# Optimization experiments

Hardware: AMD Instinct MI355X
Metric: run time of the kernel (lower is better)

Reference implementation:

```python
import jax, jax.numpy as jnp
import numpy as np

B, N, DIM, H, DH = 2, 4096, 512, 8, 64  # inner_dim = H*DH = 512


def setup_inputs() -> dict:
    key = jax.random.key(0)
    ks = jax.random.split(key, 4)
    x = jax.random.normal(ks[0], (B, N, DIM), dtype=jnp.float32)
    Wq = jax.random.normal(ks[1], (DIM, H * DH), dtype=jnp.float32) * (DIM ** -0.5)
    Wkv = jax.random.normal(ks[2], (DIM, 2 * H * DH), dtype=jnp.float32) * (DIM ** -0.5)
    Wo = jax.random.normal(ks[3], (H * DH, DIM), dtype=jnp.float32) * ((H * DH) ** -0.5)
    bo = jnp.zeros((DIM,), dtype=jnp.float32)
    return {"x": x, "Wq": Wq, "Wkv": Wkv, "Wo": Wo, "bo": bo}


def reference(x, Wq, Wkv, Wo, bo):
    scale = DH ** -0.5
    # projections (context defaults to x -> self-attention)
    q = x @ Wq
    kv = x @ Wkv
    k, v = jnp.split(kv, 2, axis=-1)
    # NOTE: original code scales q by dim_head**-0.5 in forward() AND again
    # inside attention(), i.e. an effective dim_head**-1 scaling. Faithful.
    q = q * scale
    # b n (h d) -> b h n d
    split_heads = lambda t: t.reshape(B, N, H, DH).transpose(0, 2, 1, 3)
    q, k, v = map(split_heads, (q, k, v))
    q = q * scale  # second scaling inside attention()
    sim = jnp.einsum('bhid,bhjd->bhij', q, k)  # [B,H,N,N] full score matrix
    sim = sim - jax.lax.stop_gradient(jnp.max(sim, axis=-1, keepdims=True))
    mask_value = -jnp.finfo(sim.dtype).max
    causal_mask = jnp.triu(jnp.ones((N, N), dtype=bool), k=1)
    sim = jnp.where(causal_mask, mask_value, sim)
    attn = jax.nn.softmax(sim, axis=-1)
    out = jnp.einsum('bhij,bhjd->bhid', attn, v)
    out = out.transpose(0, 2, 1, 3).reshape(B, N, H * DH)  # b h n d -> b n (h d)
    return out @ Wo + bo
```

## Files before the change

kernel.cpp:

```cpp
#include <hip/hip_runtime.h>

typedef short s16x8 __attribute__((ext_vector_type(8)));
typedef float f32x4 __attribute__((ext_vector_type(4)));
typedef unsigned short u16;
typedef unsigned int u32;

#define MFMA16(a, b, c) __builtin_amdgcn_mfma_f32_16x16x32_bf16((a), (b), (c), 0, 0, 0)

__device__ __forceinline__ u16 f2bf(float f) {
  u32 u = __float_as_uint(f);
  u += 0x7fffu + ((u >> 16) & 1u);
  return (u16)(u >> 16);
}
__device__ __forceinline__ u16 f2bf_fast(float f) {
  return (u16)((__float_as_uint(f) + 0x8000u) >> 16);
}
__device__ __forceinline__ float ex2(float x) {
  float r;
  asm("v_exp_f32 %0, %1" : "=v"(r) : "v"(x));
  return r;
}
__device__ __forceinline__ void gll(const u16* g, u16* l) {
  __builtin_amdgcn_global_load_lds((const __attribute__((address_space(1))) u32*)g,
                                   (__attribute__((address_space(3))) u32*)l, 16, 0, 0);
}

__global__ __launch_bounds__(256) void k_prep(const float* __restrict__ x,
                                              const float* __restrict__ Wq,
                                              const float* __restrict__ Wkv,
                                              const float* __restrict__ Wo,
                                              u16* __restrict__ xb,
                                              u16* __restrict__ wqkvt,
                                              u16* __restrict__ wot) {
  const int bx = blockIdx.x, t = threadIdx.x;
  if (bx < 4096) {
    int i = bx * 256 + t;
    float4 v = ((const float4*)x)[i];
    ushort4 o;
    o.x = f2bf(v.x); o.y = f2bf(v.y); o.z = f2bf(v.z); o.w = f2bf(v.w);
    ((ushort4*)xb)[i] = o;
    return;
  }
  __shared__ u16 tl[64 * 66];
  const float* src; u16* dst; int N, kb, nb;
  if (bx < 4160)      { int tb = bx - 4096; src = Wq;  dst = wqkvt;          N = 512;  kb = tb >> 3; nb = tb & 7; }
  else if (bx < 4288) { int tb = bx - 4160; src = Wkv; dst = wqkvt + 262144; N = 1024; kb = tb >> 4; nb = tb & 15; }
  else                { int tb = bx - 4288; src = Wo;  dst = wot;            N = 512;  kb = tb >> 3; nb = tb & 7; }
#pragma unroll
  for (int it = 0; it < 4; ++it) {
    int idx = it * 256 + t;
    int kl = idx >> 4, nc = idx & 15;
    float4 v = *(const float4*)(src + (kb * 64 + kl) * N + nb * 64 + nc * 4);
    u16* p = &tl[kl * 66 + nc * 4];
    p[0] = f2bf(v.x); p[1] = f2bf(v.y); p[2] = f2bf(v.z); p[3] = f2bf(v.w);
  }
  __syncthreads();
#pragma unroll
  for (int it = 0; it < 2; ++it) {
    int idx = it * 256 + t;
    int nl = idx >> 3, kc = idx & 7;
    u16 tmp[8];
#pragma unroll
    for (int j = 0; j < 8; ++j) tmp[j] = tl[(kc * 8 + j) * 66 + nl];
    *(s16x8*)(dst + (nb * 64 + nl) * 512 + kb * 64 + kc * 8) = *(const s16x8*)tmp;
  }
}

__global__ __launch_bounds__(256, 2) void k_gemm_qkv(
    const u16* __restrict__ A, const u16* __restrict__ Bt,
    u16* __restrict__ Qb, u16* __restrict__ Kb, u16* __restrict__ Vt) {
  __shared__ __align__(16) u16 As[8192], Bs[8192];
  const int t = threadIdx.x, w = t >> 6, l = t & 63, quad = l >> 4, lr = l & 15;
  const int bm = blockIdx.x, bn = blockIdx.y;
  const int wm = (w >> 1) * 64, wn = (w & 1) * 64;
  const f32x4 fz = {0.f, 0.f, 0.f, 0.f};
  f32x4 acc[4][4];
#pragma unroll
  for (int i = 0; i < 4; ++i)
#pragma unroll
    for (int j = 0; j < 4; ++j) acc[i][j] = fz;
  const u16* Ag = A + bm * 128 * 512;
  const u16* Bg = Bt + bn * 128 * 512;
  for (int kk = 0; kk < 8; ++kk) {
    __syncthreads();
#pragma unroll
    for (int i = 0; i < 4; ++i) {
      int ci = w * 256 + i * 64 + l;
      int row = ci >> 3, cb = ci & 7;
      int off = row * 512 + kk * 64 + ((cb ^ (row & 7)) << 3);
      gll(Ag + off, &As[w * 2048 + i * 512]);
      gll(Bg + off, &Bs[w * 2048 + i * 512]);
    }
    __syncthreads();
    s16x8 af[4][2], bf[4][2];
#pragma unroll
    for (int x2 = 0; x2 < 4; ++x2)
#pragma unroll
      for (int c = 0; c < 2; ++c) {
        int sw = ((c * 4 + quad) ^ (lr & 7)) << 3;
        af[x2][c] = *(const s16x8*)&As[(wm + x2 * 16 + lr) * 64 + sw];
        bf[x2][c] = *(const s16x8*)&Bs[(wn + x2 * 16 + lr) * 64 + sw];
      }
#pragma unroll
    for (int c = 0; c < 2; ++c)
#pragma unroll
      for (int ti = 0; ti < 4; ++ti)
#pragma unroll
        for (int tj = 0; tj < 4; ++tj)
          acc[ti][tj] = MFMA16(af[ti][c], bf[tj][c], acc[ti][tj]);
  }
  const int buf = (bn * 128) >> 9;
  const float QS = 0.0225421107f;
#pragma unroll
  for (int ti = 0; ti < 4; ++ti)
#pragma unroll
    for (int tj = 0; tj < 4; ++tj) {
      int col = bn * 128 + wn + tj * 16 + lr;
      int hd = col & 511, h = hd >> 6, d = hd & 63;
      int row0 = bm * 128 + wm + ti * 16 + quad * 4;
      int b = row0 >> 12, n0 = row0 & 4095;
      long base = (long)(b * 8 + h) * 262144;
      if (buf == 0) {
#pragma unroll
        for (int r = 0; r < 4; ++r) Qb[base + (long)(n0 + r) * 64 + d] = f2bf(acc[ti][tj][r] * QS);
      } else if (buf == 1) {
#pragma unroll
        for (int r = 0; r < 4; ++r) Kb[base + (long)(n0 + r) * 64 + d] = f2bf(acc[ti][tj][r]);
      } else {
        ushort4 pk;
        pk.x = f2bf(acc[ti][tj][0]); pk.y = f2bf(acc[ti][tj][1]);
        pk.z = f2bf(acc[ti][tj][2]); pk.w = f2bf(acc[ti][tj][3]);
        *(ushort4*)&Vt[base + (long)d * 4096 + n0] = pk;
      }
    }
}

__global__ __launch_bounds__(256, 2) void k_gemm_out(
    const u16* __restrict__ A, const u16* __restrict__ Bt,
    const float* __restrict__ bias, float* __restrict__ out) {
  __shared__ __align__(16) u16 As[8192], Bs[8192];
  const int t = threadIdx.x, w = t >> 6, l = t & 63, quad = l >> 4, lr = l & 15;
  const int bm = blockIdx.x, bn = blockIdx.y;
  const int wm = (w >> 1) * 64, wn = (w & 1) * 64;
  const f32x4 fz = {0.f, 0.f, 0.f, 0.f};
  f32x4 acc[4][4];
#pragma unroll
  for (int i = 0; i < 4; ++i)
#pragma unroll
    for (int j = 0; j < 4; ++j) acc[i][j] = fz;
  const u16* Ag = A + bm * 128 * 512;
  const u16* Bg = Bt + bn * 128 * 512;
  for (int kk = 0; kk < 8; ++kk) {
    __syncthreads();
#pragma unroll
    for (int i = 0; i < 4; ++i) {
      int ci = w * 256 + i * 64 + l;
      int row = ci >> 3, cb = ci & 7;
      int off = row * 512 + kk * 64 + ((cb ^ (row & 7)) << 3);
      gll(Ag + off, &As[w * 2048 + i * 512]);
      gll(Bg + off, &Bs[w * 2048 + i * 512]);
    }
    __syncthreads();
    s16x8 af[4][2], bf[4][2];
#pragma unroll
    for (int x2 = 0; x2 < 4; ++x2)
#pragma unroll
      for (int c = 0; c < 2; ++c) {
        int sw = ((c * 4 + quad) ^ (lr & 7)) << 3;
        af[x2][c] = *(const s16x8*)&As[(wm + x2 * 16 + lr) * 64 + sw];
        bf[x2][c] = *(const s16x8*)&Bs[(wn + x2 * 16 + lr) * 64 + sw];
      }
#pragma unroll
    for (int c = 0; c < 2; ++c)
#pragma unroll
      for (int ti = 0; ti < 4; ++ti)
#pragma unroll
        for (int tj = 0; tj < 4; ++tj)
          acc[ti][tj] = MFMA16(af[ti][c], bf[tj][c], acc[ti][tj]);
  }
#pragma unroll
  for (int ti = 0; ti < 4; ++ti)
#pragma unroll
    for (int tj = 0; tj < 4; ++tj) {
      int col = bn * 128 + wn + tj * 16 + lr;
      float bb = bias[col];
#pragma unroll
      for (int r = 0; r < 4; ++r) {
        int row = bm * 128 + wm + ti * 16 + quad * 4 + r;
        out[(long)row * 512 + col] = acc[ti][tj][r] + bb;
      }
    }
}

__global__ __launch_bounds__(256, 2) void k_attn(
    const u16* __restrict__ Qb, const u16* __restrict__ Kb,
    const u16* __restrict__ Vt, u16* __restrict__ Ob) {
  __shared__ __align__(16) u16 lds[25600];
  const int t = threadIdx.x, w = t >> 6, l = t & 63, quad = l >> 4, lr = l & 15;
  const int bid = blockIdx.x;
  const int qt = 31 - (bid >> 4), bh = bid & 15;
  const u16* Qh = Qb + (long)bh * 262144;
  const u16* Kh = Kb + (long)bh * 262144;
  const u16* Vh = Vt + (long)bh * 262144;
  const int rw0 = qt * 128 + w * 32;
  const int jend = 2 * qt + 1;
  s16x8 qf[2][2];
#pragma unroll
  for (int mt = 0; mt < 2; ++mt)
#pragma unroll
    for (int c = 0; c < 2; ++c)
      qf[mt][c] = *(const s16x8*)(Qh + (rw0 + mt * 16 + lr) * 64 + c * 32 + quad * 8);
  const f32x4 fz = {0.f, 0.f, 0.f, 0.f};
  f32x4 o[2][4];
#pragma unroll
  for (int mt = 0; mt < 2; ++mt)
#pragma unroll
    for (int nt = 0; nt < 4; ++nt) o[mt][nt] = fz;
  float m_r[2][4], l_r[2][4];
#pragma unroll
  for (int mt = 0; mt < 2; ++mt)
#pragma unroll
    for (int r = 0; r < 4; ++r) { m_r[mt][r] = -3.0e38f; l_r[mt][r] = 0.f; }
  u16* P = &lds[16384 + w * 2304];
  const int ci0 = w * 128 + l;

  {
#pragma unroll
    for (int i = 0; i < 2; ++i) {
      int ci = ci0 + i * 64, row = ci >> 3, cb = ci & 7;
      int sw = (cb ^ (row & 7)) << 3;
      gll(Kh + row * 64 + sw, &lds[(w * 2 + i) * 512]);
      gll(Vh + row * 4096 + sw, &lds[8192 + (w * 2 + i) * 512]);
    }
  }
  for (int jt = 0; jt <= jend; ++jt) {
    const int buf = jt & 1;
    __syncthreads();
    if (jt < jend) {
      const u16* Ksrc = Kh + (jt + 1) * 4096;
      const u16* Vsrc = Vh + (jt + 1) * 64;
      const int nb = buf ^ 1;
#pragma unroll
      for (int i = 0; i < 2; ++i) {
        int ci = ci0 + i * 64, row = ci >> 3, cb = ci & 7;
        int sw = (cb ^ (row & 7)) << 3;
        gll(Ksrc + row * 64 + sw, &lds[nb * 4096 + (w * 2 + i) * 512]);
        gll(Vsrc + row * 4096 + sw, &lds[8192 + nb * 4096 + (w * 2 + i) * 512]);
      }
    }
    if (jt * 64 >= rw0 + 32) continue;
    const u16* Ks = &lds[buf * 4096];
    const u16* Vs = &lds[8192 + buf * 4096];
    f32x4 s[2][4];
#pragma unroll
    for (int mt = 0; mt < 2; ++mt)
#pragma unroll
      for (int nt = 0; nt < 4; ++nt) s[mt][nt] = fz;
#pragma unroll
    for (int c = 0; c < 2; ++c) {
      s16x8 kbf[4];
#pragma unroll
      for (int nt = 0; nt < 4; ++nt)
        kbf[nt] = *(const s16x8*)&Ks[(nt * 16 + lr) * 64 + (((c * 4 + quad) ^ (lr & 7)) << 3)];
#pragma unroll
      for (int mt = 0; mt < 2; ++mt)
#pragma unroll
        for (int nt = 0; nt < 4; ++nt)
          s[mt][nt] = MFMA16(qf[mt][c], kbf[nt], s[mt][nt]);
    }
    const bool dg = (jt * 64 + 63 > rw0);
#pragma unroll
    for (int mt = 0; mt < 2; ++mt) {
      if (dg) {
        int rloc = rw0 - jt * 64 + mt * 16 + quad * 4;
#pragma unroll
        for (int nt = 0; nt < 4; ++nt)
#pragma unroll
          for (int r = 0; r < 4; ++r)
            if (nt * 16 + lr > rloc + r) s[mt][nt][r] = -1e30f;
      }
      float al[4];
#pragma unroll
      for (int r = 0; r < 4; ++r) {
        float lm = fmaxf(fmaxf(s[mt][0][r], s[mt][1][r]), fmaxf(s[mt][2][r], s[mt][3][r]));
        lm = fmaxf(lm, __shfl_xor(lm, 1));
        lm = fmaxf(lm, __shfl_xor(lm, 2));
        lm = fmaxf(lm, __shfl_xor(lm, 4));
        lm = fmaxf(lm, __shfl_xor(lm, 8));
        float mn = fmaxf(m_r[mt][r], lm);
        al[r] = ex2(m_r[mt][r] - mn);
        m_r[mt][r] = mn;
      }
#pragma unroll
      for (int nt = 0; nt < 4; ++nt)
#pragma unroll
        for (int r = 0; r < 4; ++r) s[mt][nt][r] = ex2(s[mt][nt][r] - m_r[mt][r]);
#pragma unroll
      for (int r = 0; r < 4; ++r) {
        float ts = (s[mt][0][r] + s[mt][1][r]) + (s[mt][2][r] + s[mt][3][r]);
        ts += __shfl_xor(ts, 1);
        ts += __shfl_xor(ts, 2);
        ts += __shfl_xor(ts, 4);
        ts += __shfl_xor(ts, 8);
        l_r[mt][r] = l_r[mt][r] * al[r] + ts;
      }
#pragma unroll
      for (int nt = 0; nt < 4; ++nt)
#pragma unroll
        for (int r = 0; r < 4; ++r)
          P[(mt * 16 + quad * 4 + r) * 72 + nt * 16 + lr] = f2bf_fast(s[mt][nt][r]);
#pragma unroll
      for (int nt = 0; nt < 4; ++nt)
#pragma unroll
        for (int r = 0; r < 4; ++r) o[mt][nt][r] *= al[r];
    }
#pragma unroll
    for (int c = 0; c < 2; ++c) {
      s16x8 ap[2], bv[4];
#pragma unroll
      for (int mt = 0; mt < 2; ++mt)
        ap[mt] = *(const s16x8*)&P[(mt * 16 + lr) * 72 + c * 32 + quad * 8];
#pragma unroll
      for (int nt = 0; nt < 4; ++nt)
        bv[nt] = *(const s16x8*)&Vs[(nt * 16 + lr) * 64 + (((c * 4 + quad) ^ (lr & 7)) << 3)];
#pragma unroll
      for (int mt = 0; mt < 2; ++mt)
#pragma unroll
        for (int nt = 0; nt < 4; ++nt)
          o[mt][nt] = MFMA16(ap[mt], bv[nt], o[mt][nt]);
    }
  }
#pragma unroll
  for (int mt = 0; mt < 2; ++mt) {
    float inv[4];
#pragma unroll
    for (int r = 0; r < 4; ++r) inv[r] = 1.0f / l_r[mt][r];
#pragma unroll
    for (int nt = 0; nt < 4; ++nt)
#pragma unroll
      for (int r = 0; r < 4; ++r)
        P[(mt * 16 + quad * 4 + r) * 72 + nt * 16 + lr] = f2bf(o[mt][nt][r] * inv[r]);
  }
  const int b = bh >> 3, h = bh & 7;
  const int row2 = l >> 1, half = l & 1;
  long gbase = (long)(b * 4096 + rw0 + row2) * 512 + h * 64 + half * 32;
  const u16* ps = &P[row2 * 72 + half * 32];
#pragma unroll
  for (int k = 0; k < 4; ++k)
    *(s16x8*)(Ob + gbase + k * 8) = *(const s16x8*)(ps + k * 8);
}

extern "C" void kernel_launch(void* const* d_in, const int* in_sizes, int n_in,
                              void* d_out, int out_size, void* d_ws, size_t ws_size,
                              hipStream_t stream) {
  const float* x   = (const float*)d_in[0];
  const float* Wq  = (const float*)d_in[1];
  const float* Wkv = (const float*)d_in[2];
  const float* Wo  = (const float*)d_in[3];
  const float* bo  = (const float*)d_in[4];
  float* out = (float*)d_out;
  char* ws = (char*)d_ws;
  u16* xbf   = (u16*)(ws + (0ull << 20));
  u16* wqkvt = (u16*)(ws + (8ull << 20));
  u16* wot   = (u16*)(ws + (10ull << 20));
  u16* Qb    = (u16*)(ws + (11ull << 20));
  u16* Kb    = (u16*)(ws + (19ull << 20));
  u16* Vtb   = (u16*)(ws + (27ull << 20));
  u16* Ob    = (u16*)(ws + (35ull << 20));

  k_prep<<<4352, 256, 0, stream>>>(x, Wq, Wkv, Wo, xbf, wqkvt, wot);
  k_gemm_qkv<<<dim3(64, 12), 256, 0, stream>>>(xbf, wqkvt, Qb, Kb, Vtb);
  k_attn<<<512, 256, 0, stream>>>(Qb, Kb, Vtb, Ob);
  k_gemm_out<<<dim3(64, 4), 256, 0, stream>>>(Ob, wot, bo, out);
}
```

Baseline: 266.3 us.

## Split causal attention KV range into chunks and combine partial results

Adds a split-KV flash attention path. Each query tile's causal KV range is cut into chunks of 16 KV tiles processed by separate blocks, which write partial outputs plus max and sum statistics. A combine kernel then merges them with log-sum-exp weights. This targets load imbalance and the long tail from late query tiles that have long KV loops, at the cost of an extra kernel, extra global traffic for the partials, and a larger workspace requirement; the old monolithic kernel remains as the fallback when the workspace is too small.

```diff
diff --git a/kernel.cpp b/kernel.cpp
--- a/kernel.cpp
+++ b/kernel.cpp
@@ -14,6 +14,9 @@
 }
 __device__ __forceinline__ u16 f2bf_fast(float f) {
   return (u16)((__float_as_uint(f) + 0x8000u) >> 16);
+}
+__device__ __forceinline__ float bf2f(u16 u) {
+  return __uint_as_float(((u32)u) << 16);
 }
 __device__ __forceinline__ float ex2(float x) {
   float r;
@@ -192,7 +195,214 @@
     }
 }
 
-__global__ __launch_bounds__(256, 2) void k_attn(
+__global__ __launch_bounds__(256, 2) void k_attn_split(
+    const u16* __restrict__ Qb, const u16* __restrict__ Kb,
+    const u16* __restrict__ Vt, u16* __restrict__ pO,
+    float* __restrict__ pM, float* __restrict__ pL) {
+  const int bid = blockIdx.x;
+  const int qt = 31 - (bid >> 6), rem = bid & 63, bh = rem >> 2, c = rem & 3;
+  const int nc = (qt >> 3) + 1;
+  if (c >= nc) return;
+  __shared__ __align__(16) u16 lds[25600];
+  const int t = threadIdx.x, w = t >> 6, l = t & 63, quad = l >> 4, lr = l & 15;
+  const u16* Qh = Qb + (long)bh * 262144;
+  const u16* Kh = Kb + (long)bh * 262144;
+  const u16* Vh = Vt + (long)bh * 262144;
+  const int rw0 = qt * 128 + w * 32;
+  const int jstart = c * 16;
+  const int jendx = min(jstart + 16, 2 * qt + 2);
+  s16x8 qf[2][2];
+#pragma unroll
+  for (int mt = 0; mt < 2; ++mt)
+#pragma unroll
+    for (int cc = 0; cc < 2; ++cc)
+      qf[mt][cc] = *(const s16x8*)(Qh + (rw0 + mt * 16 + lr) * 64 + cc * 32 + quad * 8);
+  const f32x4 fz = {0.f, 0.f, 0.f, 0.f};
+  f32x4 o[2][4];
+#pragma unroll
+  for (int mt = 0; mt < 2; ++mt)
+#pragma unroll
+    for (int nt = 0; nt < 4; ++nt) o[mt][nt] = fz;
+  float m_r[2][4], l_r[2][4];
+#pragma unroll
+  for (int mt = 0; mt < 2; ++mt)
+#pragma unroll
+    for (int r = 0; r < 4; ++r) { m_r[mt][r] = -3.0e38f; l_r[mt][r] = 0.f; }
+  u16* P = &lds[16384 + w * 2304];
+  const int ci0 = w * 128 + l;
+
+  {
+    const u16* Ksrc = Kh + jstart * 4096;
+    const u16* Vsrc = Vh + jstart * 64;
+    const int b0 = jstart & 1;
+#pragma unroll
+    for (int i = 0; i < 2; ++i) {
+      int ci = ci0 + i * 64, row = ci >> 3, cb = ci & 7;
+      int sw = (cb ^ (row & 7)) << 3;
+      gll(Ksrc + row * 64 + sw, &lds[b0 * 4096 + (w * 2 + i) * 512]);
+      gll(Vsrc + row * 4096 + sw, &lds[8192 + b0 * 4096 + (w * 2 + i) * 512]);
+    }
+  }
+  for (int jt = jstart; jt < jendx; ++jt) {
+    const int buf = jt & 1;
+    __syncthreads();
+    if (jt + 1 < jendx) {
+      const u16* Ksrc = Kh + (jt + 1) * 4096;
+      const u16* Vsrc = Vh + (jt + 1) * 64;
+      const int nb = buf ^ 1;
+#pragma unroll
+      for (int i = 0; i < 2; ++i) {
+        int ci = ci0 + i * 64, row = ci >> 3, cb = ci & 7;
+        int sw = (cb ^ (row & 7)) << 3;
+        gll(Ksrc + row * 64 + sw, &lds[nb * 4096 + (w * 2 + i) * 512]);
+        gll(Vsrc + row * 4096 + sw, &lds[8192 + nb * 4096 + (w * 2 + i) * 512]);
+      }
+    }
+    if (jt * 64 >= rw0 + 32) continue;
+    const u16* Ks = &lds[buf * 4096];
+    const u16* Vs = &lds[8192 + buf * 4096];
+    f32x4 s[2][4];
+#pragma unroll
+    for (int mt = 0; mt < 2; ++mt)
+#pragma unroll
+      for (int nt = 0; nt < 4; ++nt) s[mt][nt] = fz;
+#pragma unroll
+    for (int cc = 0; cc < 2; ++cc) {
+      s16x8 kbf[4];
+#pragma unroll
+      for (int nt = 0; nt < 4; ++nt)
+        kbf[nt] = *(const s16x8*)&Ks[(nt * 16 + lr) * 64 + (((cc * 4 + quad) ^ (lr & 7)) << 3)];
+#pragma unroll
+      for (int mt = 0; mt < 2; ++mt)
+#pragma unroll
+        for (int nt = 0; nt < 4; ++nt)
+          s[mt][nt] = MFMA16(qf[mt][cc], kbf[nt], s[mt][nt]);
+    }
+    const bool dg = (jt * 64 + 63 > rw0);
+#pragma unroll
+    for (int mt = 0; mt < 2; ++mt) {
+      if (dg) {
+        int rloc = rw0 - jt * 64 + mt * 16 + quad * 4;
+#pragma unroll
+        for (int nt = 0; nt < 4; ++nt)
+#pragma unroll
+          for (int r = 0; r < 4; ++r)
+            if (nt * 16 + lr > rloc + r) s[mt][nt][r] = -1e30f;
+      }
+      float al[4];
+#pragma unroll
+      for (int r = 0; r < 4; ++r) {
+        float lm = fmaxf(fmaxf(s[mt][0][r], s[mt][1][r]), fmaxf(s[mt][2][r], s[mt][3][r]));
+        lm = fmaxf(lm, __shfl_xor(lm, 1));
+        lm = fmaxf(lm, __shfl_xor(lm, 2));
+        lm = fmaxf(lm, __shfl_xor(lm, 4));
+        lm = fmaxf(lm, __shfl_xor(lm, 8));
+        float mn = fmaxf(m_r[mt][r], lm);
+        al[r] = ex2(m_r[mt][r] - mn);
+        m_r[mt][r] = mn;
+      }
+#pragma unroll
+      for (int nt = 0; nt < 4; ++nt)
+#pragma unroll
+        for (int r = 0; r < 4; ++r) s[mt][nt][r] = ex2(s[mt][nt][r] - m_r[mt][r]);
+#pragma unroll
+      for (int r = 0; r < 4; ++r) {
+        float ts = (s[mt][0][r] + s[mt][1][r]) + (s[mt][2][r] + s[mt][3][r]);
+        ts += __shfl_xor(ts, 1);
+        ts += __shfl_xor(ts, 2);
+        ts += __shfl_xor(ts, 4);
+        ts += __shfl_xor(ts, 8);
+        l_r[mt][r] = l_r[mt][r] * al[r] + ts;
+      }
+#pragma unroll
+      for (int nt = 0; nt < 4; ++nt)
+#pragma unroll
+        for (int r = 0; r < 4; ++r)
+          P[(mt * 16 + quad * 4 + r) * 72 + nt * 16 + lr] = f2bf_fast(s[mt][nt][r]);
+#pragma unroll
+      for (int nt = 0; nt < 4; ++nt)
+#pragma unroll
+        for (int r = 0; r < 4; ++r) o[mt][nt][r] *= al[r];
+    }
+#pragma unroll
+    for (int cc = 0; cc < 2; ++cc) {
+      s16x8 ap[2], bv[4];
+#pragma unroll
+      for (int mt = 0; mt < 2; ++mt)
+        ap[mt] = *(const s16x8*)&P[(mt * 16 + lr) * 72 + cc * 32 + quad * 8];
+#pragma unroll
+      for (int nt = 0; nt < 4; ++nt)
+        bv[nt] = *(const s16x8*)&Vs[(nt * 16 + lr) * 64 + (((cc * 4 + quad) ^ (lr & 7)) << 3)];
+#pragma unroll
+      for (int mt = 0; mt < 2; ++mt)
+#pragma unroll
+        for (int nt = 0; nt < 4; ++nt)
+          o[mt][nt] = MFMA16(ap[mt], bv[nt], o[mt][nt]);
+    }
+  }
+  const int pidx = (bh * 32 + qt) * 4 + c;
+#pragma unroll
+  for (int mt = 0; mt < 2; ++mt) {
+    if (lr == 0) {
+#pragma unroll
+      for (int r = 0; r < 4; ++r) {
+        int rl = w * 32 + mt * 16 + quad * 4 + r;
+        pM[pidx * 128 + rl] = m_r[mt][r];
+        pL[pidx * 128 + rl] = l_r[mt][r];
+      }
+    }
+#pragma unroll
+    for (int nt = 0; nt < 4; ++nt)
+#pragma unroll
+      for (int r = 0; r < 4; ++r)
+        P[(mt * 16 + quad * 4 + r) * 72 + nt * 16 + lr] = f2bf(o[mt][nt][r]);
+  }
+  const int row2 = l >> 1, half = l & 1;
+  long gbase = (long)pidx * 8192 + (w * 32 + row2) * 64 + half * 32;
+  const u16* ps = &P[row2 * 72 + half * 32];
+#pragma unroll
+  for (int k = 0; k < 4; ++k)
+    *(s16x8*)(pO + gbase + k * 8) = *(const s16x8*)(ps + k * 8);
+}
+
+__global__ __launch_bounds__(256) void k_comb(const u16* __restrict__ pO,
+                                              const float* __restrict__ pM,
+                                              const float* __restrict__ pL,
+                                              u16* __restrict__ Ob) {
+  const int bid = blockIdx.x, t = threadIdx.x;
+  const int bh = bid >> 5, qt = bid & 31;
+  const int nc = (qt >> 3) + 1;
+  const int row = t >> 1, half = t & 1;
+  const int pbase = (bh * 32 + qt) * 4;
+  float M = -3.0e38f;
+  for (int c = 0; c < nc; ++c) M = fmaxf(M, pM[(pbase + c) * 128 + row]);
+  float L = 0.f;
+  float acc[32];
+#pragma unroll
+  for (int d = 0; d < 32; ++d) acc[d] = 0.f;
+  for (int c = 0; c < nc; ++c) {
+    float wgt = ex2(pM[(pbase + c) * 128 + row] - M);
+    L += pL[(pbase + c) * 128 + row] * wgt;
+    const u16* src = pO + (long)(pbase + c) * 8192 + row * 64 + half * 32;
+#pragma unroll
+    for (int k = 0; k < 4; ++k) {
+      s16x8 v = *(const s16x8*)(src + k * 8);
+#pragma unroll
+      for (int j = 0; j < 8; ++j) acc[k * 8 + j] += wgt * bf2f((u16)v[j]);
+    }
+  }
+  float inv = 1.0f / L;
+  u16 tmp[32];
+#pragma unroll
+  for (int d = 0; d < 32; ++d) tmp[d] = f2bf(acc[d] * inv);
+  const int b = bh >> 3, h = bh & 7;
+  long gbase = (long)(b * 4096 + qt * 128 + row) * 512 + h * 64 + half * 32;
+#pragma unroll
+  for (int k = 0; k < 4; ++k)
+    *(s16x8*)(Ob + gbase + k * 8) = *(const s16x8*)(tmp + k * 8);
+}
+
+__global__ __launch_bounds__(256, 2) void k_attn_mono(
     const u16* __restrict__ Qb, const u16* __restrict__ Kb,
     const u16* __restrict__ Vt, u16* __restrict__ Ob) {
   __shared__ __align__(16) u16 lds[25600];
@@ -223,7 +433,6 @@
     for (int r = 0; r < 4; ++r) { m_r[mt][r] = -3.0e38f; l_r[mt][r] = 0.f; }
   u16* P = &lds[16384 + w * 2304];
   const int ci0 = w * 128 + l;
-
   {
 #pragma unroll
     for (int i = 0; i < 2; ++i) {
@@ -360,16 +569,26 @@
   const float* bo  = (const float*)d_in[4];
   float* out = (float*)d_out;
   char* ws = (char*)d_ws;
-  u16* xbf   = (u16*)(ws + (0ull << 20));
-  u16* wqkvt = (u16*)(ws + (8ull << 20));
-  u16* wot   = (u16*)(ws + (10ull << 20));
-  u16* Qb    = (u16*)(ws + (11ull << 20));
-  u16* Kb    = (u16*)(ws + (19ull << 20));
-  u16* Vtb   = (u16*)(ws + (27ull << 20));
-  u16* Ob    = (u16*)(ws + (35ull << 20));
+  const size_t MB = 1048576;
+  u16* wot   = (u16*)(ws);
+  u16* wqkvt = (u16*)(ws + MB / 2);
+  u16* Qb    = (u16*)(ws + 2 * MB);
+  u16* Kb    = (u16*)(ws + 10 * MB);
+  u16* Vtb   = (u16*)(ws + 18 * MB);
+  u16* Ob    = (u16*)(ws + 26 * MB);
+  u16* xbf   = (u16*)(ws + 34 * MB);
+  u16* pO    = (u16*)(ws + 34 * MB);
+  float* pM  = (float*)(ws + 34 * MB + 33554432);
+  float* pL  = (float*)(ws + 34 * MB + 33554432 + 1048576);
+  const size_t needed = 34 * MB + 33554432 + 2 * 1048576;
 
   k_prep<<<4352, 256, 0, stream>>>(x, Wq, Wkv, Wo, xbf, wqkvt, wot);
   k_gemm_qkv<<<dim3(64, 12), 256, 0, stream>>>(xbf, wqkvt, Qb, Kb, Vtb);
-  k_attn<<<512, 256, 0, stream>>>(Qb, Kb, Vtb, Ob);
+  if (ws_size >= needed) {
+    k_attn_split<<<2048, 256, 0, stream>>>(Qb, Kb, Vtb, pO, pM, pL);
+    k_comb<<<512, 256, 0, stream>>>(pO, pM, pL, Ob);
+  } else {
+    k_attn_mono<<<512, 256, 0, stream>>>(Qb, Kb, Vtb, Ob);
+  }
   k_gemm_out<<<dim3(64, 4), 256, 0, stream>>>(Ob, wot, bo, out);
 }
```

Result: slower. 273.5 us (+2.7%).
